# Optimization experiments

Hardware: AMD Instinct MI355X
Metric: run time of the kernel (lower is better)

## Reference

```python
import jax, jax.numpy as jnp
import numpy as np

N = 50000        # nodes
E = 800000       # edges (avg degree 16)
F = 64           # num_features
G = 128          # number of graphs in the batch
NOUT = 1         # n_output


def setup_inputs() -> dict:
    key = jax.random.key(0)
    ks = jax.random.split(key, 9)
    x = jax.random.normal(ks[0], (N, F), dtype=jnp.float32)
    edge_index = jax.random.randint(ks[1], (2, E), 0, N, dtype=jnp.int64)
    batch = jnp.sort(jax.random.randint(ks[2], (N,), 0, G, dtype=jnp.int64))
    W1 = jax.random.normal(ks[3], (F, F), dtype=jnp.float32) * 0.1
    b1 = jnp.zeros((F,), dtype=jnp.float32)
    W2 = jax.random.normal(ks[4], (F, 2 * F), dtype=jnp.float32) * 0.1
    b2 = jnp.zeros((2 * F,), dtype=jnp.float32)
    fcW = jax.random.normal(ks[5], (2 * F, NOUT), dtype=jnp.float32) * 0.1
    fcb = jnp.zeros((NOUT,), dtype=jnp.float32)
    return {"x": x, "edge_index": edge_index, "batch": batch,
            "W1": W1, "b1": b1, "W2": W2, "b2": b2, "fcW": fcW, "fcb": fcb}


def reference(x, edge_index, batch, W1, b1, W2, b2, fcW, fcb):
    n = x.shape[0]
    # PyG GCNConv: add self-loops, symmetric normalization D^-1/2 (A+I) D^-1/2
    loop = jnp.arange(n, dtype=edge_index.dtype)
    src = jnp.concatenate([edge_index[0], loop])  # [E+N]
    dst = jnp.concatenate([edge_index[1], loop])  # [E+N]
    deg = jax.ops.segment_sum(jnp.ones_like(dst, dtype=x.dtype), dst, num_segments=n)
    dinv = jnp.where(deg > 0, jax.lax.rsqrt(jnp.maximum(deg, 1.0)), 0.0)
    norm = dinv[src] * dinv[dst]                  # [E+N]

    def gcn_conv(h, W, b):
        h = h @ W                                 # [N, Fout]
        msg = h[src] * norm[:, None]              # gather + scale, [E+N, Fout]
        return jax.ops.segment_sum(msg, dst, num_segments=n) + b

    h1 = jax.nn.relu(gcn_conv(x, W1, b1))         # [N, F]
    h2 = jax.nn.relu(gcn_conv(h1, W2, b2))        # [N, 2F]

    # global mean pool per graph (dropout is identity in eval)
    counts = jax.ops.segment_sum(jnp.ones((n,), x.dtype), batch, num_segments=G)
    pooled = jax.ops.segment_sum(h2, batch, num_segments=G)
    pooled = pooled / jnp.maximum(counts, 1.0)[:, None]  # [G, 2F]

    out = pooled @ fcW + fcb                      # [G, NOUT]
    return out.reshape(1, -1)                     # [1, G*NOUT]
```

## Files before the change

kernel.cpp:

```cpp
#include <hip/hip_runtime.h>
#include <hip/hip_bf16.h>

typedef __hip_bfloat16 bf16;

static __device__ __forceinline__ float loadF(const void* p, long long i, int f32){
  return f32 ? ((const float*)p)[i] : __bfloat162float(((const bf16*)p)[i]);
}
static __device__ __forceinline__ int loadI(const void* p, long long i, int i64){
  return i64 ? (int)((const long long*)p)[i] : ((const int*)p)[i];
}
static __device__ __forceinline__ unsigned short f2bf(float f){
  unsigned u = __float_as_uint(f);
  return (unsigned short)((u + 0x7FFFu + ((u>>16)&1u)) >> 16);
}
static __device__ __forceinline__ float bf2f(unsigned v){
  return __uint_as_float(v<<16);
}

#define CAP 4096
#define LB_EDGES 4096

__global__ void k_init(const unsigned int* __restrict__ xw, const unsigned int* __restrict__ eiw,
                       int* __restrict__ flags, int* __restrict__ gcursor, int nbuckets,
                       float* __restrict__ S, int gn){
  int i = blockIdx.x*256 + threadIdx.x;
  if(i < nbuckets) gcursor[i] = 0;
  if(i < gn) S[i] = 0.f;
  if(blockIdx.x == 0){
    __shared__ int s1, s2;
    if(threadIdx.x==0){ s1=0; s2=0; }
    __syncthreads();
    unsigned w = xw[threadIdx.x];
    int e = (int)((w>>7)&0xFFu);
    if(e>=110 && e<=135) atomicAdd(&s1, 1);
    if(eiw[2*threadIdx.x+1] != 0u) atomicAdd(&s2, 1);
    __syncthreads();
    if(threadIdx.x==0){
      flags[0] = (s1 < 128) ? 1 : 0;
      flags[1] = (s2 < 128) ? 1 : 0;
    }
  }
}

__global__ __launch_bounds__(256) void k_logbuild(const void* __restrict__ ei, int E, int N,
                                                  const int* __restrict__ flags,
                                                  int* __restrict__ gcursor,
                                                  unsigned int* __restrict__ log, int nbuckets){
  __shared__ unsigned int stash[LB_EDGES];
  __shared__ int hcnt[1024];
  __shared__ int hbase[1024];
  int t = threadIdx.x;
  for(int b=t; b<nbuckets; b+=256) hcnt[b] = 0;
  __syncthreads();
  int i64 = flags[1];
  long long e0 = (long long)blockIdx.x*LB_EDGES;
  int cnt = (int)(((long long)E - e0) < LB_EDGES ? ((long long)E - e0) : LB_EDGES);
  for(int k=t; k<cnt; k+=256){
    long long e = e0 + k;
    int s = loadI(ei, e, i64);                 s = min(max(s,0), N-1);
    int d = loadI(ei, (long long)E + e, i64);  d = min(max(d,0), N-1);
    unsigned p = (((unsigned)d)<<16) | (unsigned)s;
    stash[k] = p;
    atomicAdd(&hcnt[d>>6], 1);
  }
  __syncthreads();
  for(int b=t; b<nbuckets; b+=256){
    int c = hcnt[b];
    hbase[b] = (c>0) ? atomicAdd(&gcursor[b], c) : 0;
    hcnt[b] = 0;
  }
  __syncthreads();
  for(int k=t; k<cnt; k+=256){
    unsigned p = stash[k];
    int b = (int)(p>>22);
    int pos = hbase[b] + atomicAdd(&hcnt[b], 1);
    if(pos < CAP) log[(long long)b*CAP + pos] = p;
  }
}

__global__ __launch_bounds__(256) void k_bsortg0(const unsigned int* __restrict__ log,
                                                 const int* __restrict__ gcursor,
                                                 unsigned short* __restrict__ csr,
                                                 int* __restrict__ beg, int* __restrict__ endv,
                                                 float* __restrict__ dinv,
                                                 const void* __restrict__ x, const int* __restrict__ flags,
                                                 unsigned short* __restrict__ g0, int N){
  __shared__ int hist[64];
  __shared__ int cur[64];
  __shared__ float dloc[64];
  int b = blockIdx.x, t = threadIdx.x;
  if(t < 64) hist[t] = 0;
  __syncthreads();
  int n = min(gcursor[b], CAP);
  const unsigned int* L = log + (long long)b*CAP;
  for(int j=t; j<n; j+=256) atomicAdd(&hist[(L[j]>>16)&63], 1);
  __syncthreads();
  if(t < 64){
    int v = hist[t];
    int inc = v;
    #pragma unroll
    for(int o=1; o<64; o<<=1){
      int u = __shfl_up(inc, o);
      if(t >= o) inc += u;
    }
    int excl = inc - v;
    cur[t] = excl;
    float dv = rsqrtf((float)(v + 1));
    dloc[t] = dv;
    int node = b*64 + t;
    if(node < N){
      int base = b*CAP + excl;
      beg[node]  = base;
      endv[node] = base + v;
      dinv[node] = dv;
    }
  }
  __syncthreads();
  unsigned short* C = csr + (long long)b*CAP;
  for(int j=t; j<n; j+=256){
    unsigned p = L[j];
    int l = (int)((p>>16)&63u);
    int pos = atomicAdd(&cur[l], 1);
    C[pos] = (unsigned short)(p & 0xFFFFu);
  }
  int f32 = flags[0];
  long long base = (long long)b*64*64;
  for(int i=t; i<4096; i+=256){
    int nl = i>>6;
    int node = b*64 + nl;
    if(node < N) g0[base + i] = f2bf(loadF(x, base + i, f32) * dloc[nl]);
  }
}

__global__ __launch_bounds__(256) void k_agg(const unsigned short* __restrict__ g,
                                             const unsigned short* __restrict__ csr,
                                             const int* __restrict__ beg, const int* __restrict__ endv,
                                             const float* __restrict__ dinv,
                                             unsigned int* __restrict__ out32, int N){
  int node = blockIdx.x*4 + (threadIdx.x>>6);
  int lane = threadIdx.x&63;
  if(node >= N) return;
  int half = lane>>5, fl = lane&31;
  const unsigned int* G32 = (const unsigned int*)g;
  int j = beg[node], e = endv[node];
  float2 a0={0.f,0.f}, a1={0.f,0.f}, a2={0.f,0.f}, a3={0.f,0.f};
  float2 a4={0.f,0.f}, a5={0.f,0.f}, a6={0.f,0.f}, a7={0.f,0.f};
  for(; j+16<=e; j+=16){
    int s0 = csr[j +  0 + half];
    int s1 = csr[j +  2 + half];
    int s2 = csr[j +  4 + half];
    int s3 = csr[j +  6 + half];
    int s4 = csr[j +  8 + half];
    int s5 = csr[j + 10 + half];
    int s6 = csr[j + 12 + half];
    int s7 = csr[j + 14 + half];
    unsigned v0 = G32[(long long)s0*32 + fl];
    unsigned v1 = G32[(long long)s1*32 + fl];
    unsigned v2 = G32[(long long)s2*32 + fl];
    unsigned v3 = G32[(long long)s3*32 + fl];
    unsigned v4 = G32[(long long)s4*32 + fl];
    unsigned v5 = G32[(long long)s5*32 + fl];
    unsigned v6 = G32[(long long)s6*32 + fl];
    unsigned v7 = G32[(long long)s7*32 + fl];
    a0.x += bf2f(v0 & 0xFFFFu); a0.y += bf2f(v0 >> 16);
    a1.x += bf2f(v1 & 0xFFFFu); a1.y += bf2f(v1 >> 16);
    a2.x += bf2f(v2 & 0xFFFFu); a2.y += bf2f(v2 >> 16);
    a3.x += bf2f(v3 & 0xFFFFu); a3.y += bf2f(v3 >> 16);
    a4.x += bf2f(v4 & 0xFFFFu); a4.y += bf2f(v4 >> 16);
    a5.x += bf2f(v5 & 0xFFFFu); a5.y += bf2f(v5 >> 16);
    a6.x += bf2f(v6 & 0xFFFFu); a6.y += bf2f(v6 >> 16);
    a7.x += bf2f(v7 & 0xFFFFu); a7.y += bf2f(v7 >> 16);
  }
  for(; j+8<=e; j+=8){
    int s0 = csr[j + 0 + half];
    int s1 = csr[j + 2 + half];
    int s2 = csr[j + 4 + half];
    int s3 = csr[j + 6 + half];
    unsigned v0 = G32[(long long)s0*32 + fl];
    unsigned v1 = G32[(long long)s1*32 + fl];
    unsigned v2 = G32[(long long)s2*32 + fl];
    unsigned v3 = G32[(long long)s3*32 + fl];
    a0.x += bf2f(v0 & 0xFFFFu); a0.y += bf2f(v0 >> 16);
    a1.x += bf2f(v1 & 0xFFFFu); a1.y += bf2f(v1 >> 16);
    a2.x += bf2f(v2 & 0xFFFFu); a2.y += bf2f(v2 >> 16);
    a3.x += bf2f(v3 & 0xFFFFu); a3.y += bf2f(v3 >> 16);
  }
  for(; j+2<=e; j+=2){
    int s = csr[j + half];
    unsigned v = G32[(long long)s*32 + fl];
    a0.x += bf2f(v & 0xFFFFu); a0.y += bf2f(v >> 16);
  }
  if(j < e && half == 0){
    int s = csr[j];
    unsigned v = G32[(long long)s*32 + fl];
    a0.x += bf2f(v & 0xFFFFu); a0.y += bf2f(v >> 16);
  }
  float sx = ((a0.x+a1.x)+(a2.x+a3.x)) + ((a4.x+a5.x)+(a6.x+a7.x));
  float sy = ((a0.y+a1.y)+(a2.y+a3.y)) + ((a4.y+a5.y)+(a6.y+a7.y));
  sx += __shfl_xor(sx, 32, 64);
  sy += __shfl_xor(sy, 32, 64);
  unsigned sv = G32[(long long)node*32 + fl];
  float dv = dinv[node];
  sx = (sx + bf2f(sv & 0xFFFFu)) * dv;
  sy = (sy + bf2f(sv >> 16)) * dv;
  if(half == 0)
    out32[(long long)node*32 + fl] = (unsigned)f2bf(sx) | ((unsigned)f2bf(sy) << 16);
}

__global__ __launch_bounds__(256) void k_gemm1(const unsigned int* __restrict__ A32, const void* __restrict__ W,
                                               const void* __restrict__ b, const int* __restrict__ flags,
                                               const float* __restrict__ dinv, unsigned short* __restrict__ out, int N){
  __shared__ float Ws[64*64];
  __shared__ float xs[128*65];
  int f32 = flags[0];
  int tid = threadIdx.x;
  for(int i=tid;i<4096;i+=256) Ws[i] = loadF(W, i, f32);
  int row0 = blockIdx.x*128;
  for(int i=tid;i<4096;i+=256){
    int r = i>>5, kd = i&31;
    int gr = row0 + r;
    unsigned v = (gr<N) ? A32[(long long)gr*32 + kd] : 0u;
    xs[r*65 + 2*kd    ] = bf2f(v & 0xFFFFu);
    xs[r*65 + 2*kd + 1] = bf2f(v >> 16);
  }
  __syncthreads();
  int cg = tid&15, rg = tid>>4;
  int col_g = cg*4, row_g = rg*8;
  float acc[8][4];
  #pragma unroll
  for(int r=0;r<8;r++){ acc[r][0]=0.f; acc[r][1]=0.f; acc[r][2]=0.f; acc[r][3]=0.f; }
  for(int k=0;k<64;k++){
    float4 w = *(const float4*)&Ws[k*64 + col_g];
    float xr[8];
    #pragma unroll
    for(int r=0;r<8;r++) xr[r] = xs[(row_g+r)*65 + k];
    #pragma unroll
    for(int r=0;r<8;r++){
      acc[r][0] += xr[r]*w.x; acc[r][1] += xr[r]*w.y;
      acc[r][2] += xr[r]*w.z; acc[r][3] += xr[r]*w.w;
    }
  }
  float b0 = loadF(b, col_g,   f32), b1v = loadF(b, col_g+1, f32);
  float b2v = loadF(b, col_g+2, f32), b3 = loadF(b, col_g+3, f32);
  #pragma unroll
  for(int r=0;r<8;r++){
    int gr = row0 + row_g + r;
    if(gr<N){
      float dv = dinv[gr];
      float v0 = acc[r][0]+b0, v1 = acc[r][1]+b1v, v2 = acc[r][2]+b2v, v3 = acc[r][3]+b3;
      v0 = (v0>0.f?v0:0.f)*dv; v1 = (v1>0.f?v1:0.f)*dv;
      v2 = (v2>0.f?v2:0.f)*dv; v3 = (v3>0.f?v3:0.f)*dv;
      ushort4 st;
      st.x = f2bf(v0); st.y = f2bf(v1); st.z = f2bf(v2); st.w = f2bf(v3);
      *(ushort4*)&out[(long long)gr*64 + col_g] = st;
    }
  }
}

__global__ __launch_bounds__(256) void k_gemm2pool(const unsigned int* __restrict__ A32, const void* __restrict__ W,
                                                   const void* __restrict__ b, const void* __restrict__ fcW,
                                                   const void* __restrict__ batch, const int* __restrict__ flags,
                                                   float* __restrict__ S, int N, int NOUT){
  __shared__ float Ws[64*128];
  __shared__ float xs[128*65];
  __shared__ float Sloc[128*4];
  __shared__ int gid[128];
  int f32 = flags[0], i64 = flags[1];
  int tid = threadIdx.x;
  int row0 = blockIdx.x*128;
  for(int i=tid;i<8192;i+=256) Ws[i] = loadF(W, i, f32);
  for(int i=tid;i<4096;i+=256){
    int r = i>>5, kd = i&31;
    int gr = row0 + r;
    unsigned v = (gr<N) ? A32[(long long)gr*32 + kd] : 0u;
    xs[r*65 + 2*kd    ] = bf2f(v & 0xFFFFu);
    xs[r*65 + 2*kd + 1] = bf2f(v >> 16);
  }
  if(tid < 128){
    int node = row0 + tid;
    gid[tid] = (node < N) ? loadI(batch, node, i64) : 0;
  }
  for(int i=tid;i<512;i+=256) Sloc[i] = 0.f;
  __syncthreads();
  int cg = tid&15, rg = tid>>4;
  int c0 = cg*4, c1 = 64 + cg*4, row_g = rg*8;
  float acc[8][8];
  #pragma unroll
  for(int r=0;r<8;r++)
    #pragma unroll
    for(int c=0;c<8;c++) acc[r][c]=0.f;
  for(int k=0;k<64;k++){
    float4 w0 = *(const float4*)&Ws[k*128 + c0];
    float4 w1 = *(const float4*)&Ws[k*128 + c1];
    float xr[8];
    #pragma unroll
    for(int r=0;r<8;r++) xr[r] = xs[(row_g+r)*65 + k];
    #pragma unroll
    for(int r=0;r<8;r++){
      acc[r][0] += xr[r]*w0.x; acc[r][1] += xr[r]*w0.y;
      acc[r][2] += xr[r]*w0.z; acc[r][3] += xr[r]*w0.w;
      acc[r][4] += xr[r]*w1.x; acc[r][5] += xr[r]*w1.y;
      acc[r][6] += xr[r]*w1.z; acc[r][7] += xr[r]*w1.w;
    }
  }
  #pragma unroll
  for(int c=0;c<8;c++){
    int col = (c<4) ? (c0+c) : (c1+c-4);
    float bb = loadF(b, col, f32);
    #pragma unroll
    for(int r=0;r<8;r++){ float z = acc[r][c]+bb; acc[r][c] = z>0.f?z:0.f; }
  }
  int nv = N - row0; nv = nv < 128 ? nv : 128;
  if(nv <= 0) return;
  int gmin = gid[0], gmax = gid[nv-1];
  bool ldsOK = (NOUT <= 4) && (gmax - gmin < 128);
  for(int o=0;o<NOUT;o++){
    float fw[8];
    #pragma unroll
    for(int c=0;c<8;c++){
      int col = (c<4) ? (c0+c) : (c1+c-4);
      fw[c] = loadF(fcW, (long long)col*NOUT + o, f32);
    }
    #pragma unroll
    for(int r=0;r<8;r++){
      float z = acc[r][0]*fw[0] + acc[r][1]*fw[1] + acc[r][2]*fw[2] + acc[r][3]*fw[3]
              + acc[r][4]*fw[4] + acc[r][5]*fw[5] + acc[r][6]*fw[6] + acc[r][7]*fw[7];
      #pragma unroll
      for(int m=1;m<16;m<<=1) z += __shfl_xor(z, m, 64);
      int nl = row_g + r;
      if(cg==0 && nl < nv){
        int gg = gid[nl];
        if(ldsOK) atomicAdd(&Sloc[(gg-gmin)*NOUT + o], z);
        else      atomicAdd(&S[(long long)gg*NOUT + o], z);
      }
    }
  }
  if(ldsOK){
    __syncthreads();
    int nbin = (gmax - gmin + 1)*NOUT;
    for(int i=tid; i<nbin; i+=256){
      float v = Sloc[i];
      if(v != 0.f){
        int bin = i / NOUT, o = i - bin*NOUT;
        atomicAdd(&S[(long long)(gmin+bin)*NOUT + o], v);
      }
    }
  }
}

static __device__ __forceinline__ int lower_bound_batch(const void* batch, int N, int key, int i64){
  int lo = 0, hi = N;
  while(lo < hi){ int mid = (lo+hi)>>1; if(loadI(batch, mid, i64) < key) lo = mid+1; else hi = mid; }
  return lo;
}

__global__ void k_final2(const float* __restrict__ S, const void* __restrict__ batch, int N,
                         const int* __restrict__ flags, const void* __restrict__ fcb,
                         void* __restrict__ out, int G, int NOUT){
  int f32 = flags[0], i64 = flags[1];
  int g = blockIdx.x*256 + threadIdx.x;
  if(g >= G) return;
  int c = lower_bound_batch(batch, N, g+1, i64) - lower_bound_batch(batch, N, g, i64);
  float inv = 1.f / (float)(c > 0 ? c : 1);
  for(int o=0;o<NOUT;o++){
    float r = S[(long long)g*NOUT+o]*inv + loadF(fcb, o, f32);
    if(f32) ((float*)out)[g*NOUT+o] = r;
    else    ((unsigned short*)out)[g*NOUT+o] = f2bf(r);
  }
}

extern "C" void kernel_launch(void* const* d_in, const int* in_sizes, int n_in,
                              void* d_out, int out_size, void* d_ws, size_t ws_size,
                              hipStream_t stream) {
  const void* x    = d_in[0];
  const void* ei   = d_in[1];
  const void* batch= d_in[2];
  const void* W1   = d_in[3];
  const void* b1   = d_in[4];
  const void* W2   = d_in[5];
  const void* b2   = d_in[6];
  const void* fcW  = d_in[7];
  const void* fcb  = d_in[8];

  const int N = in_sizes[0] / 64;
  const int E = in_sizes[1] / 2;
  const int NOUT = in_sizes[8];
  const int G = out_size / NOUT;
  const int nbuckets = (N + 63) >> 6;

  size_t off = 0;
  auto alloc = [&](size_t bytes) -> char* {
    char* p = (char*)d_ws + off;
    off += (bytes + 511) & ~(size_t)511;
    return p;
  };
  int*   flags   = (int*)  alloc(512);
  int*   gcursor = (int*)  alloc((size_t)nbuckets*4);
  float* dinv    = (float*)alloc((size_t)N*4);
  int*   beg     = (int*)  alloc((size_t)N*4);
  int*   endv    = (int*)  alloc((size_t)N*4);
  float* S       = (float*)alloc((size_t)G*NOUT*4);
  unsigned int*   log  = (unsigned int*)  alloc((size_t)nbuckets*CAP*4);
  unsigned short* csr  = (unsigned short*)alloc((size_t)nbuckets*CAP*2);
  unsigned short* g0   = (unsigned short*)alloc((size_t)N*64*2);
  unsigned short* g1   = (unsigned short*)alloc((size_t)N*64*2);
  unsigned int*   aBuf = (unsigned int*)  alloc((size_t)N*32*4);
  (void)ws_size; (void)n_in;

  int initgrid = (nbuckets > G*NOUT ? nbuckets : G*NOUT);

  k_init    <<<(initgrid+255)/256, 256, 0, stream>>>((const unsigned int*)x, (const unsigned int*)ei,
                                                     flags, gcursor, nbuckets, S, G*NOUT);
  k_logbuild<<<(E+LB_EDGES-1)/LB_EDGES, 256, 0, stream>>>(ei, E, N, flags, gcursor, log, nbuckets);
  k_bsortg0 <<<nbuckets,      256, 0, stream>>>(log, gcursor, csr, beg, endv, dinv, x, flags, g0, N);

  k_agg     <<<(N+3)/4,       256, 0, stream>>>(g0, csr, beg, endv, dinv, aBuf, N);
  k_gemm1   <<<(N+127)/128,   256, 0, stream>>>(aBuf, W1, b1, flags, dinv, g1, N);
  k_agg     <<<(N+3)/4,       256, 0, stream>>>(g1, csr, beg, endv, dinv, aBuf, N);
  k_gemm2pool<<<(N+127)/128,  256, 0, stream>>>(aBuf, W2, b2, fcW, batch, flags, S, N, NOUT);

  k_final2  <<<(G+255)/256,   256, 0, stream>>>(S, batch, N, flags, fcb, d_out, G, NOUT);
}
```

Baseline: 212.8 us.

## Split gather features into two 64-byte planes and pad CSR rows to multiples of four

Stores the bf16 feature matrices g0/g1 as two feature-half planes (16 words per node each), with a zero dummy row at index N. The aggregation kernel now runs twice as many blocks, one plane per block, and each wave gathers four edges at a time with 16 lanes per edge. CSR rows are padded to a multiple of four with the dummy node, which removes the tail branches. The intent is a smaller per-plane working set for better cache hit rates and simpler loops, at the cost of reading csr/beg/end twice and some padded-edge gathers.

```diff
diff --git a/kernel.cpp b/kernel.cpp
--- a/kernel.cpp
+++ b/kernel.cpp
@@ -20,13 +20,21 @@
 #define CAP 4096
 #define LB_EDGES 4096
 
+
 __global__ void k_init(const unsigned int* __restrict__ xw, const unsigned int* __restrict__ eiw,
                        int* __restrict__ flags, int* __restrict__ gcursor, int nbuckets,
-                       float* __restrict__ S, int gn){
+                       float* __restrict__ S, int gn,
+                       unsigned int* __restrict__ g0, unsigned int* __restrict__ g1, int N){
   int i = blockIdx.x*256 + threadIdx.x;
   if(i < nbuckets) gcursor[i] = 0;
   if(i < gn) S[i] = 0.f;
   if(blockIdx.x == 0){
+    if(threadIdx.x < 32){
+      long long PS = (long long)(N+1)*16;
+      int p = threadIdx.x>>4, off = threadIdx.x&15;
+      g0[(long long)p*PS + (long long)N*16 + off] = 0u;
+      g1[(long long)p*PS + (long long)N*16 + off] = 0u;
+    }
     __shared__ int s1, s2;
     if(threadIdx.x==0){ s1=0; s2=0; }
     __syncthreads();
@@ -84,7 +92,7 @@
                                                  int* __restrict__ beg, int* __restrict__ endv,
                                                  float* __restrict__ dinv,
                                                  const void* __restrict__ x, const int* __restrict__ flags,
-                                                 unsigned short* __restrict__ g0, int N){
+                                                 unsigned int* __restrict__ g0, int N){
   __shared__ int hist[64];
   __shared__ int cur[64];
   __shared__ float dloc[64];
@@ -97,23 +105,25 @@
   __syncthreads();
   if(t < 64){
     int v = hist[t];
-    int inc = v;
+    int vp = (v + 3) & ~3;
+    int inc = vp;
     #pragma unroll
     for(int o=1; o<64; o<<=1){
       int u = __shfl_up(inc, o);
       if(t >= o) inc += u;
     }
-    int excl = inc - v;
+    int excl = inc - vp;
     cur[t] = excl;
     float dv = rsqrtf((float)(v + 1));
     dloc[t] = dv;
     int node = b*64 + t;
     if(node < N){
-      int base = b*CAP + excl;
-      beg[node]  = base;
-      endv[node] = base + v;
+      beg[node]  = b*CAP + excl;
+      endv[node] = b*CAP + excl + v;
       dinv[node] = dv;
     }
+    unsigned short* C = csr + (long long)b*CAP;
+    for(int q=v; q<vp; q++) C[excl+q] = (unsigned short)N;
   }
   __syncthreads();
   unsigned short* C = csr + (long long)b*CAP;
@@ -124,92 +134,70 @@
     C[pos] = (unsigned short)(p & 0xFFFFu);
   }
   int f32 = flags[0];
-  long long base = (long long)b*64*64;
-  for(int i=t; i<4096; i+=256){
-    int nl = i>>6;
+  long long PS = (long long)(N+1)*16;
+  long long xbase = (long long)b*64*64;
+  for(int i=t; i<2048; i+=256){
+    int nl = i>>5, fd = i&31;
     int node = b*64 + nl;
-    if(node < N) g0[base + i] = f2bf(loadF(x, base + i, f32) * dloc[nl]);
-  }
-}
-
-__global__ __launch_bounds__(256) void k_agg(const unsigned short* __restrict__ g,
+    if(node < N){
+      int p = fd>>4, off = fd&15;
+      float u0 = loadF(x, xbase + nl*64 + 2*fd,     f32) * dloc[nl];
+      float u1 = loadF(x, xbase + nl*64 + 2*fd + 1, f32) * dloc[nl];
+      g0[(long long)p*PS + (long long)node*16 + off] = (unsigned)f2bf(u0) | ((unsigned)f2bf(u1)<<16);
+    }
+  }
+}
+
+__global__ __launch_bounds__(256) void k_agg(const unsigned int* __restrict__ Gt,
                                              const unsigned short* __restrict__ csr,
                                              const int* __restrict__ beg, const int* __restrict__ endv,
                                              const float* __restrict__ dinv,
-                                             unsigned int* __restrict__ out32, int N){
-  int node = blockIdx.x*4 + (threadIdx.x>>6);
+                                             unsigned int* __restrict__ out32, int N, int nbpp){
+  int plane = (blockIdx.x >= nbpp) ? 1 : 0;
+  int node = (blockIdx.x - plane*nbpp)*4 + (threadIdx.x>>6);
+  if(node >= N) return;
   int lane = threadIdx.x&63;
-  if(node >= N) return;
-  int half = lane>>5, fl = lane&31;
-  const unsigned int* G32 = (const unsigned int*)g;
+  int fl = lane&15, eo = lane>>4;
+  long long PS = (long long)(N+1)*16;
+  const unsigned int* G = Gt + (long long)plane*PS;
   int j = beg[node], e = endv[node];
-  float2 a0={0.f,0.f}, a1={0.f,0.f}, a2={0.f,0.f}, a3={0.f,0.f};
-  float2 a4={0.f,0.f}, a5={0.f,0.f}, a6={0.f,0.f}, a7={0.f,0.f};
-  for(; j+16<=e; j+=16){
-    int s0 = csr[j +  0 + half];
-    int s1 = csr[j +  2 + half];
-    int s2 = csr[j +  4 + half];
-    int s3 = csr[j +  6 + half];
-    int s4 = csr[j +  8 + half];
-    int s5 = csr[j + 10 + half];
-    int s6 = csr[j + 12 + half];
-    int s7 = csr[j + 14 + half];
-    unsigned v0 = G32[(long long)s0*32 + fl];
-    unsigned v1 = G32[(long long)s1*32 + fl];
-    unsigned v2 = G32[(long long)s2*32 + fl];
-    unsigned v3 = G32[(long long)s3*32 + fl];
-    unsigned v4 = G32[(long long)s4*32 + fl];
-    unsigned v5 = G32[(long long)s5*32 + fl];
-    unsigned v6 = G32[(long long)s6*32 + fl];
-    unsigned v7 = G32[(long long)s7*32 + fl];
-    a0.x += bf2f(v0 & 0xFFFFu); a0.y += bf2f(v0 >> 16);
-    a1.x += bf2f(v1 & 0xFFFFu); a1.y += bf2f(v1 >> 16);
-    a2.x += bf2f(v2 & 0xFFFFu); a2.y += bf2f(v2 >> 16);
-    a3.x += bf2f(v3 & 0xFFFFu); a3.y += bf2f(v3 >> 16);
-    a4.x += bf2f(v4 & 0xFFFFu); a4.y += bf2f(v4 >> 16);
-    a5.x += bf2f(v5 & 0xFFFFu); a5.y += bf2f(v5 >> 16);
-    a6.x += bf2f(v6 & 0xFFFFu); a6.y += bf2f(v6 >> 16);
-    a7.x += bf2f(v7 & 0xFFFFu); a7.y += bf2f(v7 >> 16);
-  }
-  for(; j+8<=e; j+=8){
-    int s0 = csr[j + 0 + half];
-    int s1 = csr[j + 2 + half];
-    int s2 = csr[j + 4 + half];
-    int s3 = csr[j + 6 + half];
-    unsigned v0 = G32[(long long)s0*32 + fl];
-    unsigned v1 = G32[(long long)s1*32 + fl];
-    unsigned v2 = G32[(long long)s2*32 + fl];
-    unsigned v3 = G32[(long long)s3*32 + fl];
-    a0.x += bf2f(v0 & 0xFFFFu); a0.y += bf2f(v0 >> 16);
-    a1.x += bf2f(v1 & 0xFFFFu); a1.y += bf2f(v1 >> 16);
-    a2.x += bf2f(v2 & 0xFFFFu); a2.y += bf2f(v2 >> 16);
-    a3.x += bf2f(v3 & 0xFFFFu); a3.y += bf2f(v3 >> 16);
-  }
-  for(; j+2<=e; j+=2){
-    int s = csr[j + half];
-    unsigned v = G32[(long long)s*32 + fl];
-    a0.x += bf2f(v & 0xFFFFu); a0.y += bf2f(v >> 16);
-  }
-  if(j < e && half == 0){
-    int s = csr[j];
-    unsigned v = G32[(long long)s*32 + fl];
-    a0.x += bf2f(v & 0xFFFFu); a0.y += bf2f(v >> 16);
-  }
-  float sx = ((a0.x+a1.x)+(a2.x+a3.x)) + ((a4.x+a5.x)+(a6.x+a7.x));
-  float sy = ((a0.y+a1.y)+(a2.y+a3.y)) + ((a4.y+a5.y)+(a6.y+a7.y));
-  sx += __shfl_xor(sx, 32, 64);
-  sy += __shfl_xor(sy, 32, 64);
-  unsigned sv = G32[(long long)node*32 + fl];
-  float dv = dinv[node];
-  sx = (sx + bf2f(sv & 0xFFFFu)) * dv;
-  sy = (sy + bf2f(sv >> 16)) * dv;
-  if(half == 0)
-    out32[(long long)node*32 + fl] = (unsigned)f2bf(sx) | ((unsigned)f2bf(sy) << 16);
+  int ep = j + ((e - j + 3) & ~3);
+  float2 c0={0.f,0.f}, c1={0.f,0.f}, c2={0.f,0.f}, c3={0.f,0.f};
+  for(; j+16<=ep; j+=16){
+    int s0 = csr[j      + eo];
+    int s1 = csr[j + 4  + eo];
+    int s2 = csr[j + 8  + eo];
+    int s3 = csr[j + 12 + eo];
+    unsigned v0 = G[(long long)s0*16 + fl];
+    unsigned v1 = G[(long long)s1*16 + fl];
+    unsigned v2 = G[(long long)s2*16 + fl];
+    unsigned v3 = G[(long long)s3*16 + fl];
+    c0.x += bf2f(v0 & 0xFFFFu); c0.y += bf2f(v0 >> 16);
+    c1.x += bf2f(v1 & 0xFFFFu); c1.y += bf2f(v1 >> 16);
+    c2.x += bf2f(v2 & 0xFFFFu); c2.y += bf2f(v2 >> 16);
+    c3.x += bf2f(v3 & 0xFFFFu); c3.y += bf2f(v3 >> 16);
+  }
+  for(; j<ep; j+=4){
+    int s = csr[j + eo];
+    unsigned v = G[(long long)s*16 + fl];
+    c0.x += bf2f(v & 0xFFFFu); c0.y += bf2f(v >> 16);
+  }
+  float sx = (c0.x+c1.x)+(c2.x+c3.x);
+  float sy = (c0.y+c1.y)+(c2.y+c3.y);
+  sx += __shfl_xor(sx, 16, 64); sx += __shfl_xor(sx, 32, 64);
+  sy += __shfl_xor(sy, 16, 64); sy += __shfl_xor(sy, 32, 64);
+  if(eo == 0){
+    unsigned sv = G[(long long)node*16 + fl];
+    float dv = dinv[node];
+    float ox = (sx + bf2f(sv & 0xFFFFu)) * dv;
+    float oy = (sy + bf2f(sv >> 16)) * dv;
+    out32[(long long)node*32 + plane*16 + fl] = (unsigned)f2bf(ox) | ((unsigned)f2bf(oy) << 16);
+  }
 }
 
 __global__ __launch_bounds__(256) void k_gemm1(const unsigned int* __restrict__ A32, const void* __restrict__ W,
                                                const void* __restrict__ b, const int* __restrict__ flags,
-                                               const float* __restrict__ dinv, unsigned short* __restrict__ out, int N){
+                                               const float* __restrict__ dinv, unsigned int* __restrict__ g1, int N){
   __shared__ float Ws[64*64];
   __shared__ float xs[128*65];
   int f32 = flags[0];
@@ -242,6 +230,9 @@
   }
   float b0 = loadF(b, col_g,   f32), b1v = loadF(b, col_g+1, f32);
   float b2v = loadF(b, col_g+2, f32), b3 = loadF(b, col_g+3, f32);
+  long long PS = (long long)(N+1)*16;
+  int p = (col_g >= 32) ? 1 : 0;
+  int off = (col_g & 31) >> 1;
   #pragma unroll
   for(int r=0;r<8;r++){
     int gr = row0 + row_g + r;
@@ -250,9 +241,10 @@
       float v0 = acc[r][0]+b0, v1 = acc[r][1]+b1v, v2 = acc[r][2]+b2v, v3 = acc[r][3]+b3;
       v0 = (v0>0.f?v0:0.f)*dv; v1 = (v1>0.f?v1:0.f)*dv;
       v2 = (v2>0.f?v2:0.f)*dv; v3 = (v3>0.f?v3:0.f)*dv;
-      ushort4 st;
-      st.x = f2bf(v0); st.y = f2bf(v1); st.z = f2bf(v2); st.w = f2bf(v3);
-      *(ushort4*)&out[(long long)gr*64 + col_g] = st;
+      uint2 st;
+      st.x = (unsigned)f2bf(v0) | ((unsigned)f2bf(v1) << 16);
+      st.y = (unsigned)f2bf(v2) | ((unsigned)f2bf(v3) << 16);
+      *(uint2*)&g1[(long long)p*PS + (long long)gr*16 + off] = st;
     }
   }
 }
@@ -402,21 +394,22 @@
   float* S       = (float*)alloc((size_t)G*NOUT*4);
   unsigned int*   log  = (unsigned int*)  alloc((size_t)nbuckets*CAP*4);
   unsigned short* csr  = (unsigned short*)alloc((size_t)nbuckets*CAP*2);
-  unsigned short* g0   = (unsigned short*)alloc((size_t)N*64*2);
-  unsigned short* g1   = (unsigned short*)alloc((size_t)N*64*2);
+  unsigned int*   g0   = (unsigned int*)  alloc((size_t)(N+1)*32*4);
+  unsigned int*   g1   = (unsigned int*)  alloc((size_t)(N+1)*32*4);
   unsigned int*   aBuf = (unsigned int*)  alloc((size_t)N*32*4);
   (void)ws_size; (void)n_in;
 
   int initgrid = (nbuckets > G*NOUT ? nbuckets : G*NOUT);
+  int nbpp = (N + 3) / 4;
 
   k_init    <<<(initgrid+255)/256, 256, 0, stream>>>((const unsigned int*)x, (const unsigned int*)ei,
-                                                     flags, gcursor, nbuckets, S, G*NOUT);
+                                                     flags, gcursor, nbuckets, S, G*NOUT, g0, g1, N);
   k_logbuild<<<(E+LB_EDGES-1)/LB_EDGES, 256, 0, stream>>>(ei, E, N, flags, gcursor, log, nbuckets);
   k_bsortg0 <<<nbuckets,      256, 0, stream>>>(log, gcursor, csr, beg, endv, dinv, x, flags, g0, N);
 
-  k_agg     <<<(N+3)/4,       256, 0, stream>>>(g0, csr, beg, endv, dinv, aBuf, N);
+  k_agg     <<<2*nbpp,        256, 0, stream>>>(g0, csr, beg, endv, dinv, aBuf, N, nbpp);
   k_gemm1   <<<(N+127)/128,   256, 0, stream>>>(aBuf, W1, b1, flags, dinv, g1, N);
-  k_agg     <<<(N+3)/4,       256, 0, stream>>>(g1, csr, beg, endv, dinv, aBuf, N);
+  k_agg     <<<2*nbpp,        256, 0, stream>>>(g1, csr, beg, endv, dinv, aBuf, N, nbpp);
   k_gemm2pool<<<(N+127)/128,  256, 0, stream>>>(aBuf, W2, b2, fcW, batch, flags, S, N, NOUT);
 
   k_final2  <<<(G+255)/256,   256, 0, stream>>>(S, batch, N, flags, fcb, d_out, G, NOUT);
```

Result: slower. 232.5 us (+9.3%).
